# Kernel optimization log

Measured on AMD Instinct MI355X. Metric: run time of the kernel, lower is better.

Reference implementation:

```python
import jax, jax.numpy as jnp
import numpy as np

B, S, D = 8, 4096, 1024
MINR, MAXR = 0.9, 0.999


def setup_inputs() -> dict:
    key = jax.random.key(0)
    ks = jax.random.split(key, 10)

    def dense(k, fin, fout):
        # lecun_normal-style init for flax nn.Dense kernels
        return jax.random.normal(k, (fin, fout), jnp.float32) * (fin ** -0.5)

    x = jax.random.normal(ks[0], (B, S, D), jnp.float32)
    # RNN 'a' param: stable_init -> uniform in [min_rad, max_rad]
    a_fwd = jax.random.uniform(ks[1], (D,), jnp.float32, MINR, MAXR)
    # RGLRU 'a' param: recurrence_init
    u = jax.random.uniform(ks[2], (D,), jnp.float32)
    log_rad = 0.5 * jnp.log(u * (MAXR ** 2 - MINR ** 2) + MINR ** 2)
    a_param = jnp.log(jnp.exp(-log_rad) - 1.0)
    return {
        "x": x,
        "a_fwd": a_fwd,
        "Wf1": dense(ks[3], D, D), "bf1": jnp.zeros((D,), jnp.float32),
        "Wf2": dense(ks[4], D, D), "bf2": jnp.zeros((D,), jnp.float32),
        "Wbx": dense(ks[5], D, D), "bbx": jnp.zeros((D,), jnp.float32),
        "Wgx": dense(ks[6], D, D), "bgx": jnp.zeros((D,), jnp.float32),
        "Wga": dense(ks[7], D, D), "bga": jnp.zeros((D,), jnp.float32),
        "a_param": a_param,
        "Wb2": dense(ks[8], D, D), "bb2": jnp.zeros((D,), jnp.float32),
    }


def reference(x, a_fwd, Wf1, bf1, Wf2, bf2, Wbx, bbx, Wgx, bgx, Wga, bga,
              a_param, Wb2, bb2):
    b = x.shape[0]
    d = Wf1.shape[1]
    identity = x
    xg = jax.nn.gelu(x)  # flax nn.gelu default = tanh approximation

    # ---- forward branch: plain linear RNN  h = a*h + x_t ----
    u = xg @ Wf1 + bf1                       # [B,S,D]
    u_sf = jnp.swapaxes(u, 0, 1)             # [S,B,D]

    def step_f(h, ut):
        h = a_fwd * h + ut
        return h, h

    _, hf = jax.lax.scan(step_f, jnp.zeros((b, d), u.dtype), u_sf)
    out_f = jnp.swapaxes(hf, 0, 1) @ Wf2 + bf2

    # ---- backward branch: RG-LRU, reversed scan ----
    v = xg @ Wbx + bbx                       # [B,S,D]
    gate_x = jax.nn.sigmoid(v @ Wgx + bgx)
    gate_a = jax.nn.sigmoid(v @ Wga + bga)
    log_a = -8.0 * gate_a * jax.nn.softplus(a_param)
    a = jnp.exp(log_a)                       # [B,S,D]
    # h = a*h + sqrt(1 - a^2) * (gate_x * v)
    scaled_in = jnp.sqrt(1.0 - jnp.exp(2.0 * log_a)) * (gate_x * v)

    a_sf = jnp.swapaxes(a, 0, 1)             # [S,B,D]
    in_sf = jnp.swapaxes(scaled_in, 0, 1)    # [S,B,D]

    def step_b(h, inp):
        a_t, g_t = inp
        h = a_t * h + g_t
        return h, h

    _, hb = jax.lax.scan(step_b, jnp.zeros((b, d), v.dtype), (a_sf, in_sf),
                         reverse=True)
    out_b = jnp.swapaxes(hb, 0, 1) @ Wb2 + bb2

    return out_f + out_b + identity
```

## Files before the change

### kernel.cpp

```cpp
#include <hip/hip_runtime.h>

typedef __bf16 bf16;
typedef __bf16 bf16x4 __attribute__((ext_vector_type(4)));
typedef __bf16 bf16x8 __attribute__((ext_vector_type(8)));
typedef float floatx4 __attribute__((ext_vector_type(4)));

typedef __attribute__((address_space(1))) const void gvoid_t;
typedef __attribute__((address_space(3))) void lvoid_t;

#define B_DIM 8
#define S_DIM 4096
#define M_DIM 32768
#define CHUNK 128
#define NCHUNK 32

__device__ __forceinline__ void gload_lds16(const bf16* g, bf16* l) {
    __builtin_amdgcn_global_load_lds((gvoid_t*)g, (lvoid_t*)l, 16, 0, 0);
}

__device__ __forceinline__ float gelu_tanh(float x) {
    float x3 = x * x * x;
    return 0.5f * x * (1.0f + tanhf(0.7978845608028654f * (x + 0.044715f * x3)));
}

__device__ __forceinline__ float sigmoidf(float z) {
    return 1.0f / (1.0f + expf(-z));
}

__global__ void prep_weights(const float* __restrict__ W0, const float* __restrict__ W1,
                             const float* __restrict__ W2, const float* __restrict__ W3,
                             const float* __restrict__ W4, const float* __restrict__ W5,
                             bf16* __restrict__ T0, bf16* __restrict__ T1,
                             bf16* __restrict__ T2, bf16* __restrict__ T3,
                             bf16* __restrict__ T4, bf16* __restrict__ T5) {
    __shared__ float tile[32][33];
    int mz = blockIdx.z;
    const float* W = mz == 0 ? W0 : mz == 1 ? W1 : mz == 2 ? W2 : mz == 3 ? W3 : mz == 4 ? W4 : W5;
    bf16* T = mz == 0 ? T0 : mz == 1 ? T1 : mz == 2 ? T2 : mz == 3 ? T3 : mz == 4 ? T4 : T5;
    int tn = blockIdx.x * 32;
    int tk = blockIdx.y * 32;
    int tx = threadIdx.x & 31, ty = threadIdx.x >> 5;
#pragma unroll
    for (int i = 0; i < 4; ++i)
        tile[ty + i * 8][tx] = W[(size_t)(tk + ty + i * 8) * 1024 + tn + tx];
    __syncthreads();
#pragma unroll
    for (int i = 0; i < 4; ++i)
        T[(size_t)(tn + ty + i * 8) * 1024 + tk + tx] = (bf16)tile[tx][ty + i * 8];
}

__global__ void sp_kernel(const float* __restrict__ a_param, float* __restrict__ spbuf) {
    int d = blockIdx.x * 256 + threadIdx.x;
    spbuf[d] = log1pf(expf(a_param[d]));
}

__global__ void gelu_kernel(const float* __restrict__ x, bf16* __restrict__ xg) {
    size_t i = (size_t)blockIdx.x * 256 + threadIdx.x;
    float4 v = ((const float4*)x)[i];
    bf16 o0 = (bf16)gelu_tanh(v.x), o1 = (bf16)gelu_tanh(v.y);
    bf16 o2 = (bf16)gelu_tanh(v.z), o3 = (bf16)gelu_tanh(v.w);
    bf16x4 o = {o0, o1, o2, o3};
    ((bf16x4*)xg)[i] = o;
}

template <int PAIR>
__launch_bounds__(512, 4)
__global__ void gemm_pair(const bf16* __restrict__ A, const bf16* __restrict__ Bt,
                          bf16* __restrict__ out0, bf16* __restrict__ out1,
                          const float* __restrict__ bias0, const float* __restrict__ bias1,
                          const float* __restrict__ sp, const bf16* __restrict__ vbuf) {
    __shared__ __align__(16) bf16 lsA[2][4096];
    __shared__ __align__(16) bf16 lsB[4][4096];
    const int tid = threadIdx.x;
    const int wave = tid >> 6;
    const int lane = tid & 63;
    const int lane15 = lane & 15;
    const int quad = lane >> 4;
    const int wm = wave >> 2;
    const int wn = wave & 3;
    const int blk = blockIdx.x;
    const int xcd = blk & 7;
    const int j = blk >> 3;
    const long m0 = (long)(xcd * 32 + (j >> 3)) * 128;
    const long n0 = (long)(j & 7) * 256;
    const int sr = tid >> 3;
    const int sk8 = (tid & 7) ^ (sr & 7);
    const bf16* gA = A + (size_t)(m0 + sr) * 1024 + sk8 * 8;
    const bf16* gB = Bt + (size_t)(n0 + sr) * 1024 + sk8 * 8;

    floatx4 acc[4][4] = {};

    for (int kt = 0; kt < 16; ++kt) {
        __syncthreads();
        gload_lds16(gA + (size_t)kt * 64, &lsA[0][tid * 8]);
        gload_lds16(gA + (size_t)64 * 1024 + kt * 64, &lsA[1][tid * 8]);
#pragma unroll
        for (int i = 0; i < 4; ++i)
            gload_lds16(gB + (size_t)(i * 64) * 1024 + kt * 64, &lsB[i][tid * 8]);
        __syncthreads();
#pragma unroll
        for (int kk = 0; kk < 2; ++kk) {
            bf16x8 af[4], bfr[4];
#pragma unroll
            for (int mi = 0; mi < 4; ++mi) {
                int rl = mi * 16 + lane15;
                af[mi] = *(const bf16x8*)&lsA[wm][rl * 64 + ((kk * 4 + quad) ^ (rl & 7)) * 8];
            }
#pragma unroll
            for (int ni = 0; ni < 4; ++ni) {
                int rl = ni * 16 + lane15;
                bfr[ni] = *(const bf16x8*)&lsB[wn][rl * 64 + ((kk * 4 + quad) ^ (rl & 7)) * 8];
            }
#pragma unroll
            for (int mi = 0; mi < 4; ++mi)
#pragma unroll
                for (int ni = 0; ni < 4; ++ni)
                    acc[mi][ni] = __builtin_amdgcn_mfma_f32_16x16x32_bf16(af[mi], bfr[ni], acc[mi][ni], 0, 0, 0);
        }
    }

    const bool first = (n0 < 1024);
    bf16* outp = first ? out0 : out1;
    const float* bp = first ? bias0 : bias1;
    const long nb = first ? n0 : (n0 - 1024);
#pragma unroll
    for (int mi = 0; mi < 4; ++mi) {
#pragma unroll
        for (int ni = 0; ni < 4; ++ni) {
            floatx4 v = acc[mi][ni];
            long gn = nb + wn * 64 + ni * 16 + lane15;
#pragma unroll
            for (int r = 0; r < 4; ++r) {
                long gm = m0 + wm * 64 + mi * 16 + quad * 4 + r;
                size_t o = (size_t)gm * 1024 + gn;
                float z = v[r] + bp[gn];
                if (PAIR == 0) {
                    outp[o] = (bf16)z;
                } else {
                    if (first) {
                        outp[o] = (bf16)(-8.0f * sigmoidf(z) * sp[gn]);
                    } else {
                        outp[o] = (bf16)(sigmoidf(z) * (float)vbuf[o]);
                    }
                }
            }
        }
    }
}

__launch_bounds__(512, 4)
__global__ void gemm_cat(const bf16* __restrict__ A0, const bf16* __restrict__ A1,
                         const bf16* __restrict__ B0t, const bf16* __restrict__ B1t,
                         float* __restrict__ outf,
                         const float* __restrict__ bias0, const float* __restrict__ bias1,
                         const float* __restrict__ xres) {
    __shared__ __align__(16) bf16 lsA[2][4096];
    __shared__ __align__(16) bf16 lsB[4][4096];
    const int tid = threadIdx.x;
    const int wave = tid >> 6;
    const int lane = tid & 63;
    const int lane15 = lane & 15;
    const int quad = lane >> 4;
    const int wm = wave >> 2;
    const int wn = wave & 3;
    const int blk = blockIdx.x;
    const int xcd = blk & 7;
    const int j = blk >> 3;
    const long m0 = (long)(xcd * 32 + (j >> 2)) * 128;
    const long n0 = (long)(j & 3) * 256;
    const int sr = tid >> 3;
    const int sk8 = (tid & 7) ^ (sr & 7);

    floatx4 acc[4][4] = {};

    for (int kt = 0; kt < 32; ++kt) {
        const bf16* Ap = (kt < 16) ? A0 : A1;
        const bf16* Bp = (kt < 16) ? B0t : B1t;
        const int ko = kt & 15;
        const bf16* gA = Ap + (size_t)(m0 + sr) * 1024 + sk8 * 8 + (size_t)ko * 64;
        const bf16* gB = Bp + (size_t)(n0 + sr) * 1024 + sk8 * 8 + (size_t)ko * 64;
        __syncthreads();
        gload_lds16(gA, &lsA[0][tid * 8]);
        gload_lds16(gA + (size_t)64 * 1024, &lsA[1][tid * 8]);
#pragma unroll
        for (int i = 0; i < 4; ++i)
            gload_lds16(gB + (size_t)(i * 64) * 1024, &lsB[i][tid * 8]);
        __syncthreads();
#pragma unroll
        for (int kk = 0; kk < 2; ++kk) {
            bf16x8 af[4], bfr[4];
#pragma unroll
            for (int mi = 0; mi < 4; ++mi) {
                int rl = mi * 16 + lane15;
                af[mi] = *(const bf16x8*)&lsA[wm][rl * 64 + ((kk * 4 + quad) ^ (rl & 7)) * 8];
            }
#pragma unroll
            for (int ni = 0; ni < 4; ++ni) {
                int rl = ni * 16 + lane15;
                bfr[ni] = *(const bf16x8*)&lsB[wn][rl * 64 + ((kk * 4 + quad) ^ (rl & 7)) * 8];
            }
#pragma unroll
            for (int mi = 0; mi < 4; ++mi)
#pragma unroll
                for (int ni = 0; ni < 4; ++ni)
                    acc[mi][ni] = __builtin_amdgcn_mfma_f32_16x16x32_bf16(af[mi], bfr[ni], acc[mi][ni], 0, 0, 0);
        }
    }

#pragma unroll
    for (int mi = 0; mi < 4; ++mi) {
#pragma unroll
        for (int ni = 0; ni < 4; ++ni) {
            floatx4 v = acc[mi][ni];
            long gn = n0 + wn * 64 + ni * 16 + lane15;
#pragma unroll
            for (int r = 0; r < 4; ++r) {
                long gm = m0 + wm * 64 + mi * 16 + quad * 4 + r;
                size_t o = (size_t)gm * 1024 + gn;
                outf[o] = v[r] + bias0[gn] + bias1[gn] + xres[o];
            }
        }
    }
}

__global__ void fscan1(const bf16* __restrict__ u, const float* __restrict__ a_fwd,
                       float* __restrict__ carry) {
    int c = blockIdx.x & 31;
    int b = blockIdx.x >> 5;
    int d = threadIdx.x * 4;
    float4 a = *(const float4*)(a_fwd + d);
    const bf16* up = u + ((size_t)(b * S_DIM + c * CHUNK)) * 1024 + d;
    float h0 = 0.0f, h1 = 0.0f, h2 = 0.0f, h3 = 0.0f;
#pragma unroll 4
    for (int t = 0; t < CHUNK; ++t) {
        bf16x4 w = *(const bf16x4*)(up + (size_t)t * 1024);
        h0 = fmaf(a.x, h0, (float)w[0]);
        h1 = fmaf(a.y, h1, (float)w[1]);
        h2 = fmaf(a.z, h2, (float)w[2]);
        h3 = fmaf(a.w, h3, (float)w[3]);
    }
    float4 o = {h0, h1, h2, h3};
    *(float4*)(carry + ((size_t)c * 8 + b) * 1024 + d) = o;
}
__global__ void fscan2(const float* __restrict__ carry, const float* __restrict__ a_fwd,
                       float* __restrict__ H) {
    int idx = blockIdx.x * 256 + threadIdx.x;
    int d = idx & 1023, b = idx >> 10;
    float a = a_fwd[d];
    float aL = a;
#pragma unroll
    for (int i = 0; i < 7; ++i) aL *= aL;
    float h = 0.0f;
    for (int c = 0; c < NCHUNK; ++c) {
        size_t o = ((size_t)c * 8 + b) * 1024 + d;
        H[o] = h;
        h = fmaf(aL, h, carry[o]);
    }
}
__global__ void fscan3(const bf16* __restrict__ u, const float* __restrict__ a_fwd,
                       const float* __restrict__ H, bf16* __restrict__ hf) {
    int c = blockIdx.x & 31;
    int b = blockIdx.x >> 5;
    int d = threadIdx.x * 4;
    float4 a = *(const float4*)(a_fwd + d);
    const bf16* up = u + ((size_t)(b * S_DIM + c * CHUNK)) * 1024 + d;
    bf16* op = hf + ((size_t)(b * S_DIM + c * CHUNK)) * 1024 + d;
    float4 h = *(const float4*)(H + ((size_t)c * 8 + b) * 1024 + d);
#pragma unroll 4
    for (int t = 0; t < CHUNK; ++t) {
        bf16x4 w = *(const bf16x4*)(up + (size_t)t * 1024);
        h.x = fmaf(a.x, h.x, (float)w[0]);
        h.y = fmaf(a.y, h.y, (float)w[1]);
        h.z = fmaf(a.z, h.z, (float)w[2]);
        h.w = fmaf(a.w, h.w, (float)w[3]);
        bf16x4 ov = {(bf16)h.x, (bf16)h.y, (bf16)h.z, (bf16)h.w};
        *(bf16x4*)(op + (size_t)t * 1024) = ov;
    }
}

__global__ void bscan1(const bf16* __restrict__ la, const bf16* __restrict__ gxv,
                       float* __restrict__ BL, float* __restrict__ BP) {
    int c = blockIdx.x & 31;
    int b = blockIdx.x >> 5;
    int d = threadIdx.x * 4;
    const bf16* lap = la + ((size_t)(b * S_DIM + c * CHUNK)) * 1024 + d;
    const bf16* gp = gxv + ((size_t)(b * S_DIM + c * CHUNK)) * 1024 + d;
    float h0 = 0.0f, h1 = 0.0f, h2 = 0.0f, h3 = 0.0f;
    float s0 = 0.0f, s1 = 0.0f, s2 = 0.0f, s3 = 0.0f;
#pragma unroll 4
    for (int t = CHUNK - 1; t >= 0; --t) {
        bf16x4 lw = *(const bf16x4*)(lap + (size_t)t * 1024);
        bf16x4 gw = *(const bf16x4*)(gp + (size_t)t * 1024);
        float l0 = (float)lw[0], l1 = (float)lw[1], l2 = (float)lw[2], l3 = (float)lw[3];
        h0 = fmaf(expf(l0), h0, sqrtf(-expm1f(2.0f * l0)) * (float)gw[0]);
        h1 = fmaf(expf(l1), h1, sqrtf(-expm1f(2.0f * l1)) * (float)gw[1]);
        h2 = fmaf(expf(l2), h2, sqrtf(-expm1f(2.0f * l2)) * (float)gw[2]);
        h3 = fmaf(expf(l3), h3, sqrtf(-expm1f(2.0f * l3)) * (float)gw[3]);
        s0 += l0; s1 += l1; s2 += l2; s3 += l3;
    }
    size_t o = ((size_t)c * 8 + b) * 1024 + d;
    float4 hv = {h0, h1, h2, h3};
    float4 pv = {expf(s0), expf(s1), expf(s2), expf(s3)};
    *(float4*)(BL + o) = hv;
    *(float4*)(BP + o) = pv;
}
__global__ void bscan2(const float* __restrict__ BL, const float* __restrict__ BP,
                       float* __restrict__ R) {
    int idx = blockIdx.x * 256 + threadIdx.x;
    int d = idx & 1023, b = idx >> 10;
    float r = 0.0f;
    for (int c = NCHUNK - 1; c >= 0; --c) {
        size_t o = ((size_t)c * 8 + b) * 1024 + d;
        R[o] = r;
        r = fmaf(BP[o], r, BL[o]);
    }
}
__global__ void bscan3(const bf16* __restrict__ la, const bf16* __restrict__ gxv,
                       const float* __restrict__ R, bf16* __restrict__ hb) {
    int c = blockIdx.x & 31;
    int b = blockIdx.x >> 5;
    int d = threadIdx.x * 4;
    const bf16* lap = la + ((size_t)(b * S_DIM + c * CHUNK)) * 1024 + d;
    const bf16* gp = gxv + ((size_t)(b * S_DIM + c * CHUNK)) * 1024 + d;
    bf16* op = hb + ((size_t)(b * S_DIM + c * CHUNK)) * 1024 + d;
    float4 h = *(const float4*)(R + ((size_t)c * 8 + b) * 1024 + d);
#pragma unroll 4
    for (int t = CHUNK - 1; t >= 0; --t) {
        bf16x4 lw = *(const bf16x4*)(lap + (size_t)t * 1024);
        bf16x4 gw = *(const bf16x4*)(gp + (size_t)t * 1024);
        float l0 = (float)lw[0], l1 = (float)lw[1], l2 = (float)lw[2], l3 = (float)lw[3];
        h.x = fmaf(expf(l0), h.x, sqrtf(-expm1f(2.0f * l0)) * (float)gw[0]);
        h.y = fmaf(expf(l1), h.y, sqrtf(-expm1f(2.0f * l1)) * (float)gw[1]);
        h.z = fmaf(expf(l2), h.z, sqrtf(-expm1f(2.0f * l2)) * (float)gw[2]);
        h.w = fmaf(expf(l3), h.w, sqrtf(-expm1f(2.0f * l3)) * (float)gw[3]);
        bf16x4 ov = {(bf16)h.x, (bf16)h.y, (bf16)h.z, (bf16)h.w};
        *(bf16x4*)(op + (size_t)t * 1024) = ov;
    }
}

extern "C" void kernel_launch(void* const* d_in, const int* in_sizes, int n_in,
                              void* d_out, int out_size, void* d_ws, size_t ws_size,
                              hipStream_t stream) {
    const float* x       = (const float*)d_in[0];
    const float* a_fwd   = (const float*)d_in[1];
    const float* Wf1     = (const float*)d_in[2];
    const float* bf1     = (const float*)d_in[3];
    const float* Wf2     = (const float*)d_in[4];
    const float* bf2     = (const float*)d_in[5];
    const float* Wbx     = (const float*)d_in[6];
    const float* bbx     = (const float*)d_in[7];
    const float* Wgx     = (const float*)d_in[8];
    const float* bgx     = (const float*)d_in[9];
    const float* Wga     = (const float*)d_in[10];
    const float* bga     = (const float*)d_in[11];
    const float* a_param = (const float*)d_in[12];
    const float* Wb2     = (const float*)d_in[13];
    const float* bb2     = (const float*)d_in[14];
    float* out = (float*)d_out;
    (void)in_sizes; (void)n_in; (void)out_size; (void)ws_size;

    char* ws = (char*)d_ws;
    size_t off = 0;
    const size_t WSZ = (size_t)1024 * 1024 * 2;
    bf16* Wf1t = (bf16*)(ws + off); off += WSZ;
    bf16* Wbxt = (bf16*)(ws + off); off += WSZ;
    bf16* Wgat = (bf16*)(ws + off); off += WSZ;
    bf16* Wgxt = (bf16*)(ws + off); off += WSZ;
    bf16* Wf2t = (bf16*)(ws + off); off += WSZ;
    bf16* Wb2t = (bf16*)(ws + off); off += WSZ;
    float* spbuf = (float*)(ws + off); off += 4096;
    const size_t BSZ = (size_t)M_DIM * 1024 * 2;
    bf16* buf0 = (bf16*)(ws + off); off += BSZ;
    bf16* buf1 = (bf16*)(ws + off); off += BSZ;
    bf16* buf2 = (bf16*)(ws + off); off += BSZ;
    float* Fc = (float*)(ws + off); off += (size_t)NCHUNK * 8 * 1024 * 4;
    float* FH = (float*)(ws + off); off += (size_t)NCHUNK * 8 * 1024 * 4;
    float* BL = (float*)(ws + off); off += (size_t)NCHUNK * 8 * 1024 * 4;
    float* BP = (float*)(ws + off); off += (size_t)NCHUNK * 8 * 1024 * 4;
    float* BR = (float*)(ws + off); off += (size_t)NCHUNK * 8 * 1024 * 4;

    bf16* xg = buf0;
    bf16* hf = buf0;
    bf16* vb = buf1;
    bf16* hb = buf1;
    bf16* la = buf2;
    bf16* ub = (bf16*)d_out;
    bf16* gxv = (bf16*)d_out;

    prep_weights<<<dim3(32, 32, 6), 256, 0, stream>>>(Wf1, Wbx, Wga, Wgx, Wf2, Wb2,
                                                      Wf1t, Wbxt, Wgat, Wgxt, Wf2t, Wb2t);
    sp_kernel<<<4, 256, 0, stream>>>(a_param, spbuf);
    gelu_kernel<<<32768, 256, 0, stream>>>(x, xg);
    gemm_pair<0><<<2048, 512, 0, stream>>>(xg, Wf1t, ub, vb, bf1, bbx, nullptr, nullptr);
    fscan1<<<256, 256, 0, stream>>>(ub, a_fwd, Fc);
    fscan2<<<32, 256, 0, stream>>>(Fc, a_fwd, FH);
    fscan3<<<256, 256, 0, stream>>>(ub, a_fwd, FH, hf);
    gemm_pair<1><<<2048, 512, 0, stream>>>(vb, Wgat, la, gxv, bga, bgx, spbuf, vb);
    bscan1<<<256, 256, 0, stream>>>(la, gxv, BL, BP);
    bscan2<<<32, 256, 0, stream>>>(BL, BP, BR);
    bscan3<<<256, 256, 0, stream>>>(la, gxv, BR, hb);
    gemm_cat<<<1024, 512, 0, stream>>>(hf, hb, Wf2t, Wb2t, out, bf2, bb2, x);
}
```

Measured before the change: 1.007 ms.

## Merge forward and backward chunked scans into shared kernels with finer chunks

```diff
diff --git a/kernel.cpp b/kernel.cpp
--- a/kernel.cpp
+++ b/kernel.cpp
@@ -1,6 +1,7 @@
 #include <hip/hip_runtime.h>
 
 typedef __bf16 bf16;
+typedef __bf16 bf16x2 __attribute__((ext_vector_type(2)));
 typedef __bf16 bf16x4 __attribute__((ext_vector_type(4)));
 typedef __bf16 bf16x8 __attribute__((ext_vector_type(8)));
 typedef float floatx4 __attribute__((ext_vector_type(4)));
@@ -11,8 +12,8 @@
 #define B_DIM 8
 #define S_DIM 4096
 #define M_DIM 32768
-#define CHUNK 128
-#define NCHUNK 32
+#define CH 64
+#define NCH 64
 
 __device__ __forceinline__ void gload_lds16(const bf16* g, bf16* l) {
     __builtin_amdgcn_global_load_lds((gvoid_t*)g, (lvoid_t*)l, 16, 0, 0);
@@ -223,118 +224,118 @@
     }
 }
 
-__global__ void fscan1(const bf16* __restrict__ u, const float* __restrict__ a_fwd,
-                       float* __restrict__ carry) {
-    int c = blockIdx.x & 31;
-    int b = blockIdx.x >> 5;
-    int d = threadIdx.x * 4;
-    float4 a = *(const float4*)(a_fwd + d);
-    const bf16* up = u + ((size_t)(b * S_DIM + c * CHUNK)) * 1024 + d;
-    float h0 = 0.0f, h1 = 0.0f, h2 = 0.0f, h3 = 0.0f;
+__global__ void scan1(const bf16* __restrict__ u, const float* __restrict__ a_fwd,
+                      float* __restrict__ Fc,
+                      const bf16* __restrict__ la, const bf16* __restrict__ gxv,
+                      float* __restrict__ BL, float* __restrict__ BP) {
+    int id = blockIdx.x;
+    bool bwd = id >= 1024;
+    id &= 1023;
+    int dg = id & 1;
+    int c = (id >> 1) & 63;
+    int b = id >> 7;
+    int d = (dg * 256 + threadIdx.x) * 2;
+    size_t base = ((size_t)(b * S_DIM + c * CH)) * 1024 + d;
+    size_t co = ((size_t)c * 8 + b) * 1024 + d;
+    if (!bwd) {
+        float a0 = a_fwd[d], a1 = a_fwd[d + 1];
+        const bf16* up = u + base;
+        float h0 = 0.0f, h1 = 0.0f;
+#pragma unroll 8
+        for (int t = 0; t < CH; ++t) {
+            bf16x2 w = *(const bf16x2*)(up + (size_t)t * 1024);
+            h0 = fmaf(a0, h0, (float)w[0]);
+            h1 = fmaf(a1, h1, (float)w[1]);
+        }
+        Fc[co] = h0; Fc[co + 1] = h1;
+    } else {
+        const bf16* lap = la + base;
+        const bf16* gp = gxv + base;
+        float h0 = 0.0f, h1 = 0.0f, s0 = 0.0f, s1 = 0.0f;
 #pragma unroll 4
-    for (int t = 0; t < CHUNK; ++t) {
-        bf16x4 w = *(const bf16x4*)(up + (size_t)t * 1024);
-        h0 = fmaf(a.x, h0, (float)w[0]);
-        h1 = fmaf(a.y, h1, (float)w[1]);
-        h2 = fmaf(a.z, h2, (float)w[2]);
-        h3 = fmaf(a.w, h3, (float)w[3]);
-    }
-    float4 o = {h0, h1, h2, h3};
-    *(float4*)(carry + ((size_t)c * 8 + b) * 1024 + d) = o;
-}
-__global__ void fscan2(const float* __restrict__ carry, const float* __restrict__ a_fwd,
-                       float* __restrict__ H) {
-    int idx = blockIdx.x * 256 + threadIdx.x;
+        for (int t = CH - 1; t >= 0; --t) {
+            bf16x2 lw = *(const bf16x2*)(lap + (size_t)t * 1024);
+            bf16x2 gw = *(const bf16x2*)(gp + (size_t)t * 1024);
+            float l0 = (float)lw[0], l1 = (float)lw[1];
+            h0 = fmaf(expf(l0), h0, sqrtf(-expm1f(2.0f * l0)) * (float)gw[0]);
+            h1 = fmaf(expf(l1), h1, sqrtf(-expm1f(2.0f * l1)) * (float)gw[1]);
+            s0 += l0; s1 += l1;
+        }
+        BL[co] = h0; BL[co + 1] = h1;
+        BP[co] = expf(s0); BP[co + 1] = expf(s1);
+    }
+}
+
+__global__ void scan2(const float* __restrict__ Fc, const float* __restrict__ a_fwd,
+                      float* __restrict__ FH,
+                      const float* __restrict__ BL, const float* __restrict__ BP,
+                      float* __restrict__ BR) {
+    int bid = blockIdx.x;
+    bool bwd = bid >= 32;
+    int idx = (bid & 31) * 256 + threadIdx.x;
     int d = idx & 1023, b = idx >> 10;
-    float a = a_fwd[d];
-    float aL = a;
-#pragma unroll
-    for (int i = 0; i < 7; ++i) aL *= aL;
-    float h = 0.0f;
-    for (int c = 0; c < NCHUNK; ++c) {
-        size_t o = ((size_t)c * 8 + b) * 1024 + d;
-        H[o] = h;
-        h = fmaf(aL, h, carry[o]);
-    }
-}
-__global__ void fscan3(const bf16* __restrict__ u, const float* __restrict__ a_fwd,
-                       const float* __restrict__ H, bf16* __restrict__ hf) {
-    int c = blockIdx.x & 31;
-    int b = blockIdx.x >> 5;
-    int d = threadIdx.x * 4;
-    float4 a = *(const float4*)(a_fwd + d);
-    const bf16* up = u + ((size_t)(b * S_DIM + c * CHUNK)) * 1024 + d;
-    bf16* op = hf + ((size_t)(b * S_DIM + c * CHUNK)) * 1024 + d;
-    float4 h = *(const float4*)(H + ((size_t)c * 8 + b) * 1024 + d);
+    if (!bwd) {
+        float a = a_fwd[d];
+        float aL = a;
+#pragma unroll
+        for (int i = 0; i < 6; ++i) aL *= aL;
+        float h = 0.0f;
+        for (int c = 0; c < NCH; ++c) {
+            size_t o = ((size_t)c * 8 + b) * 1024 + d;
+            FH[o] = h;
+            h = fmaf(aL, h, Fc[o]);
+        }
+    } else {
+        float r = 0.0f;
+        for (int c = NCH - 1; c >= 0; --c) {
+            size_t o = ((size_t)c * 8 + b) * 1024 + d;
+            BR[o] = r;
+            r = fmaf(BP[o], r, BL[o]);
+        }
+    }
+}
+
+__global__ void scan3(const bf16* __restrict__ u, const float* __restrict__ a_fwd,
+                      const float* __restrict__ FH, bf16* __restrict__ hf,
+                      const bf16* __restrict__ la, const bf16* __restrict__ gxv,
+                      const float* __restrict__ BR, bf16* __restrict__ hb) {
+    int id = blockIdx.x;
+    bool bwd = id >= 1024;
+    id &= 1023;
+    int dg = id & 1;
+    int c = (id >> 1) & 63;
+    int b = id >> 7;
+    int d = (dg * 256 + threadIdx.x) * 2;
+    size_t base = ((size_t)(b * S_DIM + c * CH)) * 1024 + d;
+    size_t co = ((size_t)c * 8 + b) * 1024 + d;
+    if (!bwd) {
+        float a0 = a_fwd[d], a1 = a_fwd[d + 1];
+        const bf16* up = u + base;
+        bf16* op = hf + base;
+        float h0 = FH[co], h1 = FH[co + 1];
 #pragma unroll 4
-    for (int t = 0; t < CHUNK; ++t) {
-        bf16x4 w = *(const bf16x4*)(up + (size_t)t * 1024);
-        h.x = fmaf(a.x, h.x, (float)w[0]);
-        h.y = fmaf(a.y, h.y, (float)w[1]);
-        h.z = fmaf(a.z, h.z, (float)w[2]);
-        h.w = fmaf(a.w, h.w, (float)w[3]);
-        bf16x4 ov = {(bf16)h.x, (bf16)h.y, (bf16)h.z, (bf16)h.w};
-        *(bf16x4*)(op + (size_t)t * 1024) = ov;
-    }
-}
-
-__global__ void bscan1(const bf16* __restrict__ la, const bf16* __restrict__ gxv,
-                       float* __restrict__ BL, float* __restrict__ BP) {
-    int c = blockIdx.x & 31;
-    int b = blockIdx.x >> 5;
-    int d = threadIdx.x * 4;
-    const bf16* lap = la + ((size_t)(b * S_DIM + c * CHUNK)) * 1024 + d;
-    const bf16* gp = gxv + ((size_t)(b * S_DIM + c * CHUNK)) * 1024 + d;
-    float h0 = 0.0f, h1 = 0.0f, h2 = 0.0f, h3 = 0.0f;
-    float s0 = 0.0f, s1 = 0.0f, s2 = 0.0f, s3 = 0.0f;
+        for (int t = 0; t < CH; ++t) {
+            bf16x2 w = *(const bf16x2*)(up + (size_t)t * 1024);
+            h0 = fmaf(a0, h0, (float)w[0]);
+            h1 = fmaf(a1, h1, (float)w[1]);
+            bf16x2 ov = {(bf16)h0, (bf16)h1};
+            *(bf16x2*)(op + (size_t)t * 1024) = ov;
+        }
+    } else {
+        const bf16* lap = la + base;
+        const bf16* gp = gxv + base;
+        bf16* op = hb + base;
+        float h0 = BR[co], h1 = BR[co + 1];
 #pragma unroll 4
-    for (int t = CHUNK - 1; t >= 0; --t) {
-        bf16x4 lw = *(const bf16x4*)(lap + (size_t)t * 1024);
-        bf16x4 gw = *(const bf16x4*)(gp + (size_t)t * 1024);
-        float l0 = (float)lw[0], l1 = (float)lw[1], l2 = (float)lw[2], l3 = (float)lw[3];
-        h0 = fmaf(expf(l0), h0, sqrtf(-expm1f(2.0f * l0)) * (float)gw[0]);
-        h1 = fmaf(expf(l1), h1, sqrtf(-expm1f(2.0f * l1)) * (float)gw[1]);
-        h2 = fmaf(expf(l2), h2, sqrtf(-expm1f(2.0f * l2)) * (float)gw[2]);
-        h3 = fmaf(expf(l3), h3, sqrtf(-expm1f(2.0f * l3)) * (float)gw[3]);
-        s0 += l0; s1 += l1; s2 += l2; s3 += l3;
-    }
-    size_t o = ((size_t)c * 8 + b) * 1024 + d;
-    float4 hv = {h0, h1, h2, h3};
-    float4 pv = {expf(s0), expf(s1), expf(s2), expf(s3)};
-    *(float4*)(BL + o) = hv;
-    *(float4*)(BP + o) = pv;
-}
-__global__ void bscan2(const float* __restrict__ BL, const float* __restrict__ BP,
-                       float* __restrict__ R) {
-    int idx = blockIdx.x * 256 + threadIdx.x;
-    int d = idx & 1023, b = idx >> 10;
-    float r = 0.0f;
-    for (int c = NCHUNK - 1; c >= 0; --c) {
-        size_t o = ((size_t)c * 8 + b) * 1024 + d;
-        R[o] = r;
-        r = fmaf(BP[o], r, BL[o]);
-    }
-}
-__global__ void bscan3(const bf16* __restrict__ la, const bf16* __restrict__ gxv,
-                       const float* __restrict__ R, bf16* __restrict__ hb) {
-    int c = blockIdx.x & 31;
-    int b = blockIdx.x >> 5;
-    int d = threadIdx.x * 4;
-    const bf16* lap = la + ((size_t)(b * S_DIM + c * CHUNK)) * 1024 + d;
-    const bf16* gp = gxv + ((size_t)(b * S_DIM + c * CHUNK)) * 1024 + d;
-    bf16* op = hb + ((size_t)(b * S_DIM + c * CHUNK)) * 1024 + d;
-    float4 h = *(const float4*)(R + ((size_t)c * 8 + b) * 1024 + d);
-#pragma unroll 4
-    for (int t = CHUNK - 1; t >= 0; --t) {
-        bf16x4 lw = *(const bf16x4*)(lap + (size_t)t * 1024);
-        bf16x4 gw = *(const bf16x4*)(gp + (size_t)t * 1024);
-        float l0 = (float)lw[0], l1 = (float)lw[1], l2 = (float)lw[2], l3 = (float)lw[3];
-        h.x = fmaf(expf(l0), h.x, sqrtf(-expm1f(2.0f * l0)) * (float)gw[0]);
-        h.y = fmaf(expf(l1), h.y, sqrtf(-expm1f(2.0f * l1)) * (float)gw[1]);
-        h.z = fmaf(expf(l2), h.z, sqrtf(-expm1f(2.0f * l2)) * (float)gw[2]);
-        h.w = fmaf(expf(l3), h.w, sqrtf(-expm1f(2.0f * l3)) * (float)gw[3]);
-        bf16x4 ov = {(bf16)h.x, (bf16)h.y, (bf16)h.z, (bf16)h.w};
-        *(bf16x4*)(op + (size_t)t * 1024) = ov;
+        for (int t = CH - 1; t >= 0; --t) {
+            bf16x2 lw = *(const bf16x2*)(lap + (size_t)t * 1024);
+            bf16x2 gw = *(const bf16x2*)(gp + (size_t)t * 1024);
+            float l0 = (float)lw[0], l1 = (float)lw[1];
+            h0 = fmaf(expf(l0), h0, sqrtf(-expm1f(2.0f * l0)) * (float)gw[0]);
+            h1 = fmaf(expf(l1), h1, sqrtf(-expm1f(2.0f * l1)) * (float)gw[1]);
+            bf16x2 ov = {(bf16)h0, (bf16)h1};
+            *(bf16x2*)(op + (size_t)t * 1024) = ov;
+        }
     }
 }
 
@@ -373,11 +374,12 @@
     bf16* buf0 = (bf16*)(ws + off); off += BSZ;
     bf16* buf1 = (bf16*)(ws + off); off += BSZ;
     bf16* buf2 = (bf16*)(ws + off); off += BSZ;
-    float* Fc = (float*)(ws + off); off += (size_t)NCHUNK * 8 * 1024 * 4;
-    float* FH = (float*)(ws + off); off += (size_t)NCHUNK * 8 * 1024 * 4;
-    float* BL = (float*)(ws + off); off += (size_t)NCHUNK * 8 * 1024 * 4;
-    float* BP = (float*)(ws + off); off += (size_t)NCHUNK * 8 * 1024 * 4;
-    float* BR = (float*)(ws + off); off += (size_t)NCHUNK * 8 * 1024 * 4;
+    const size_t CSZ = (size_t)NCH * 8 * 1024 * 4;
+    float* Fc = (float*)(ws + off); off += CSZ;
+    float* FH = (float*)(ws + off); off += CSZ;
+    float* BL = (float*)(ws + off); off += CSZ;
+    float* BP = (float*)(ws + off); off += CSZ;
+    float* BR = (float*)(ws + off); off += CSZ;
 
     bf16* xg = buf0;
     bf16* hf = buf0;
@@ -385,19 +387,16 @@
     bf16* hb = buf1;
     bf16* la = buf2;
     bf16* ub = (bf16*)d_out;
-    bf16* gxv = (bf16*)d_out;
+    bf16* gxv = (bf16*)d_out + (size_t)M_DIM * 1024;
 
     prep_weights<<<dim3(32, 32, 6), 256, 0, stream>>>(Wf1, Wbx, Wga, Wgx, Wf2, Wb2,
                                                       Wf1t, Wbxt, Wgat, Wgxt, Wf2t, Wb2t);
     sp_kernel<<<4, 256, 0, stream>>>(a_param, spbuf);
     gelu_kernel<<<32768, 256, 0, stream>>>(x, xg);
     gemm_pair<0><<<2048, 512, 0, stream>>>(xg, Wf1t, ub, vb, bf1, bbx, nullptr, nullptr);
-    fscan1<<<256, 256, 0, stream>>>(ub, a_fwd, Fc);
-    fscan2<<<32, 256, 0, stream>>>(Fc, a_fwd, FH);
-    fscan3<<<256, 256, 0, stream>>>(ub, a_fwd, FH, hf);
     gemm_pair<1><<<2048, 512, 0, stream>>>(vb, Wgat, la, gxv, bga, bgx, spbuf, vb);
-    bscan1<<<256, 256, 0, stream>>>(la, gxv, BL, BP);
-    bscan2<<<32, 256, 0, stream>>>(BL, BP, BR);
-    bscan3<<<256, 256, 0, stream>>>(la, gxv, BR, hb);
+    scan1<<<2048, 256, 0, stream>>>(ub, a_fwd, Fc, la, gxv, BL, BP);
+    scan2<<<64, 256, 0, stream>>>(Fc, a_fwd, FH, BL, BP, BR);
+    scan3<<<2048, 256, 0, stream>>>(ub, a_fwd, FH, hf, la, gxv, BR, hb);
     gemm_cat<<<1024, 512, 0, stream>>>(hf, hb, Wf2t, Wb2t, out, bf2, bb2, x);
 }
```

New measurement: 978.3 us. 1.03x faster.
